# Kernel optimization log

Hardware: AMD Instinct MI355X
Metric: run time of the kernel (lower is better)

Reference implementation:

```python
import jax, jax.numpy as jnp
import numpy as np

ALPHA = 0.2          # LeakyReLU negative slope
NEG_INF = -9e15      # mask value from the original code


def setup_inputs() -> dict:
    key = jax.random.key(0)
    k1, k2, k3, k4 = jax.random.split(key, 4)
    B, N, F_in, F_out = 8, 2048, 64, 64
    x = jax.random.normal(k1, (B, N, F_in), dtype=jnp.float32)
    adj = jax.random.randint(k2, (B, N, N), 0, 2, dtype=jnp.int32)
    W = jax.random.normal(k3, (F_in, F_out), dtype=jnp.float32)
    a = jax.random.normal(k4, (2 * F_out, 1), dtype=jnp.float32)
    return {"x": x, "adj": adj, "W": W, "a": a}


def reference(x, adj, W, a):
    # h: [B, N, F_out]
    h = jnp.matmul(x, W)
    F_out = W.shape[1]
    a1 = a[:F_out, 0]   # source half of attention vector
    a2 = a[F_out:, 0]   # target half
    # e_ij = leakyrelu(h_i . a1 + h_j . a2)  -- identical math to the
    # original cat([h_i, h_j]) @ a without materializing [B,N*N,2F].
    s1 = jnp.einsum('bnf,f->bn', h, a1)  # [B, N]
    s2 = jnp.einsum('bnf,f->bn', h, a2)  # [B, N]
    e = jax.nn.leaky_relu(s1[:, :, None] + s2[:, None, :], negative_slope=ALPHA)
    masked = jnp.where(adj > 0, e, NEG_INF)
    attention = jax.nn.softmax(masked, axis=2)  # [B, N, N]
    # dropout p=0.0 / eval mode -> identity
    h_prime = jnp.matmul(attention, h)          # [B, N, F_out]
    return jax.nn.elu(h_prime)                  # concat=True branch
```

## Files before the change

### kernel.cpp

```cpp
#include <hip/hip_runtime.h>
#include <cstdint>

#define LRELU_ALPHA 0.2f
#define NEG_INF -9000000000000000.0f
#define L2E 1.4426950408889634f

typedef __bf16 bf16x8 __attribute__((ext_vector_type(8)));
typedef float floatx4 __attribute__((ext_vector_type(4)));

constexpr int Bb = 8, Nn = 2048, Ff = 64;
constexpr int SEG = 16;
constexpr int SEGJ = Nn / SEG;
constexpr int NROWS = Bb * Nn;
constexpr int LSTR2 = 136;

__device__ __forceinline__ unsigned f2bf_u(float f) {
    unsigned u = __builtin_bit_cast(unsigned, f);
    return u + 0x7FFFu + ((u >> 16) & 1u);
}
__device__ __forceinline__ unsigned short f2bf(float f) {
    return (unsigned short)(f2bf_u(f) >> 16);
}
__device__ __forceinline__ unsigned pkbf(float lo, float hi) {
    return (f2bf_u(lo) >> 16) | (f2bf_u(hi) & 0xFFFF0000u);
}

__global__ __launch_bounds__(256) void gat_pack(
    const int* __restrict__ adj, unsigned long long* __restrict__ amask)
{
    const int lane = threadIdx.x & 63;
    const int w    = threadIdx.x >> 6;
    const long long wave_id = (long long)blockIdx.x * 4 + w;
    const long long c0 = wave_id * 8;
    #pragma unroll
    for (int it = 0; it < 8; ++it) {
        const long long chunk = c0 + it;
        const int4 v = reinterpret_cast<const int4*>(adj + chunk * 256)[lane];
        const unsigned long long b0 = __ballot(v.x > 0);
        const unsigned long long b1 = __ballot(v.y > 0);
        const unsigned long long b2 = __ballot(v.z > 0);
        const unsigned long long b3 = __ballot(v.w > 0);
        if (lane == 0) {
            ulonglong2* o = reinterpret_cast<ulonglong2*>(amask + chunk * 4);
            o[0] = ulonglong2{b0, b1};
            o[1] = ulonglong2{b2, b3};
        }
    }
}

__global__ __launch_bounds__(256) void gat_prep(
    const float* __restrict__ x, const float* __restrict__ W, const float* __restrict__ a,
    unsigned short* __restrict__ hT, float* __restrict__ s1g, float* __restrict__ s2g)
{
    constexpr int STR2 = 36;
    __shared__ unsigned short hblk[64 * STR2];
    const int tid = threadIdx.x;
    const int blk = blockIdx.x;
    const int b  = blk >> 6;
    const int i0 = (blk & 63) * 32;
    const int w    = tid >> 6;
    const int lane = tid & 63;

    float wcol[64];
    #pragma unroll
    for (int k = 0; k < 64; ++k) wcol[k] = W[k * 64 + lane];
    const float a1 = a[lane], a2 = a[64 + lane];

    for (int r = 0; r < 8; ++r) {
        const int il = w * 8 + r;
        const int i  = i0 + il;
        const float* xrow = x + ((size_t)(b * Nn + i)) * 64;
        float h = 0.f;
        #pragma unroll
        for (int k = 0; k < 64; ++k) h = fmaf(xrow[k], wcol[k], h);
        float p1 = h * a1, p2 = h * a2;
        #pragma unroll
        for (int off = 32; off; off >>= 1) {
            p1 += __shfl_xor(p1, off);
            p2 += __shfl_xor(p2, off);
        }
        if (lane == 0) { s1g[b * Nn + i] = p1 * L2E; s2g[b * Nn + i] = p2 * L2E; }
        hblk[lane * STR2 + il] = f2bf(h);
    }
    __syncthreads();
    {
        const int f = tid >> 2, c = (tid & 3) * 8;
        uint4 v = *reinterpret_cast<const uint4*>(&hblk[f * STR2 + c]);
        *reinterpret_cast<uint4*>(hT + ((size_t)b * 64 + f) * Nn + i0 + c) = v;
    }
}

__global__ __launch_bounds__(256, 5) void gat_attn(
    const unsigned long long* __restrict__ amask, const unsigned short* __restrict__ hT,
    const float* __restrict__ s1g, const float* __restrict__ s2g,
    float* __restrict__ m_part, float* __restrict__ l_part, float* __restrict__ O_part)
{
    __shared__ __align__(16) char smem[64 * LSTR2 * 2];
    __shared__ float s2_lds[SEGJ];
    unsigned short* hT_lds = reinterpret_cast<unsigned short*>(smem);
    float* out_lds = reinterpret_cast<float*>(smem);

    const int tid  = threadIdx.x;
    const int blk  = blockIdx.x;
    const int seg  = blk >> 8;
    const int grp  = blk & 255;
    const int gr0  = grp * 64;
    const int b    = gr0 >> 11;
    const int i0   = gr0 & 2047;
    const int w    = tid >> 6;
    const int lane = tid & 63;
    const int fl   = lane & 15;
    const int q    = lane >> 4;

    const int i = i0 + w * 16 + fl;
    const float s1v = s1g[b * Nn + i];
    const unsigned short* hTb = hT + (size_t)b * 64 * Nn;
    const int jseg0 = seg * SEGJ;

    unsigned w32[4];
    {
        const unsigned long long* mrow =
            amask + (size_t)(b * Nn + i) * 32 + (seg >> 1) * 4;
        ulonglong2 m01 = reinterpret_cast<const ulonglong2*>(mrow)[0];
        ulonglong2 m23 = reinterpret_cast<const ulonglong2*>(mrow)[1];
        const int sh = (seg & 1) * 32 + q * 2;
        w32[0] = (unsigned)(m01.x >> sh);
        w32[1] = (unsigned)(m01.y >> sh);
        w32[2] = (unsigned)(m23.x >> sh);
        w32[3] = (unsigned)(m23.y >> sh);
    }

    #pragma unroll
    for (int k = 0; k < 4; ++k) {
        const int fr = k * 16 + (tid >> 4);
        const int c  = (tid & 15) * 8;
        uint4 v = *reinterpret_cast<const uint4*>(hTb + (size_t)fr * Nn + jseg0 + c);
        *reinterpret_cast<uint4*>(&hT_lds[fr * LSTR2 + c]) = v;
    }
    if (tid < SEGJ) s2_lds[tid] = s2g[b * Nn + jseg0 + tid];
    __syncthreads();

    float e[32];
    #pragma unroll
    for (int T = 0; T < 2; ++T) {
        #pragma unroll
        for (int H = 0; H < 2; ++H) {
            float s2v[8];
            *reinterpret_cast<float4*>(&s2v[0]) =
                *reinterpret_cast<const float4*>(&s2_lds[T * 64 + H * 32 + q * 8]);
            *reinterpret_cast<float4*>(&s2v[4]) =
                *reinterpret_cast<const float4*>(&s2_lds[T * 64 + H * 32 + q * 8 + 4]);
            #pragma unroll
            for (int jj = 0; jj < 8; ++jj) {
                float ev = s1v + s2v[jj];
                ev = fmaxf(ev, LRELU_ALPHA * ev);
                const bool on = (w32[jj & 3] >> (T * 16 + H * 8 + (jj >> 2))) & 1u;
                e[T * 16 + H * 8 + jj] = on ? ev : NEG_INF;
            }
        }
    }

    float m = e[0];
    #pragma unroll
    for (int k = 1; k < 32; ++k) m = fmaxf(m, e[k]);
    m = fmaxf(m, __shfl_xor(m, 16));
    m = fmaxf(m, __shfl_xor(m, 32));

    float l = 0.f;
    #pragma unroll
    for (int k = 0; k < 32; ++k) {
        e[k] = exp2f(e[k] - m);
        l += e[k];
    }
    l += __shfl_xor(l, 16);
    l += __shfl_xor(l, 32);

    floatx4 C[4] = {};
    #pragma unroll
    for (int T = 0; T < 2; ++T) {
        uint4 pl0, pl1;
        pl0.x = pkbf(e[T*16+0], e[T*16+1]);  pl0.y = pkbf(e[T*16+2], e[T*16+3]);
        pl0.z = pkbf(e[T*16+4], e[T*16+5]);  pl0.w = pkbf(e[T*16+6], e[T*16+7]);
        pl1.x = pkbf(e[T*16+8], e[T*16+9]);  pl1.y = pkbf(e[T*16+10], e[T*16+11]);
        pl1.z = pkbf(e[T*16+12], e[T*16+13]); pl1.w = pkbf(e[T*16+14], e[T*16+15]);
        const bf16x8 A0 = __builtin_bit_cast(bf16x8, pl0);
        const bf16x8 A1 = __builtin_bit_cast(bf16x8, pl1);
        #pragma unroll
        for (int u = 0; u < 4; ++u) {
            const bf16x8 B0 = *reinterpret_cast<const bf16x8*>(
                &hT_lds[(u * 16 + fl) * LSTR2 + T * 64 + q * 8]);
            C[u] = __builtin_amdgcn_mfma_f32_16x16x32_bf16(A0, B0, C[u], 0, 0, 0);
            const bf16x8 B1 = *reinterpret_cast<const bf16x8*>(
                &hT_lds[(u * 16 + fl) * LSTR2 + T * 64 + 32 + q * 8]);
            C[u] = __builtin_amdgcn_mfma_f32_16x16x32_bf16(A1, B1, C[u], 0, 0, 0);
        }
    }

    if (q == 0) {
        const int ri = b * Nn + i;
        m_part[seg * NROWS + ri] = m;
        l_part[seg * NROWS + ri] = l;
    }

    __syncthreads();
    #pragma unroll
    for (int u = 0; u < 4; ++u)
        #pragma unroll
        for (int r = 0; r < 4; ++r)
            out_lds[(w * 16 + q * 4 + r) * 65 + u * 16 + fl] = C[u][r];
    __syncthreads();
    {
        float* Obase = O_part + ((size_t)seg * NROWS + b * Nn + i0) * 64;
        #pragma unroll
        for (int k = 0; k < 4; ++k) {
            const int row = k * 16 + (tid >> 4);
            const int c4  = (tid & 15) * 4;
            float4 v = *reinterpret_cast<const float4*>(&out_lds[row * 65 + c4]);
            *reinterpret_cast<float4*>(&Obase[(size_t)row * 64 + c4]) = v;
        }
    }
}

__global__ __launch_bounds__(256) void gat_merge(
    const float* __restrict__ m_part, const float* __restrict__ l_part,
    const float* __restrict__ O_part, float* __restrict__ out)
{
    const int tid = threadIdx.x;
    const int ri  = blockIdx.x * 4 + (tid >> 6);
    const int f   = tid & 63;

    float mv[SEG];
    #pragma unroll
    for (int s = 0; s < SEG; ++s) mv[s] = m_part[s * NROWS + ri];
    float mstar = mv[0];
    #pragma unroll
    for (int s = 1; s < SEG; ++s) mstar = fmaxf(mstar, mv[s]);

    float lsum = 0.f, acc = 0.f;
    #pragma unroll
    for (int s = 0; s < SEG; ++s) {
        const float wgt = exp2f(mv[s] - mstar);
        lsum += l_part[s * NROWS + ri] * wgt;
        acc  += O_part[((size_t)s * NROWS + ri) * 64 + f] * wgt;
    }
    float v = acc / lsum;
    v = (v > 0.f) ? v : (exp2f(v * L2E) - 1.f);
    out[(size_t)ri * 64 + f] = v;
}

extern "C" void kernel_launch(void* const* d_in, const int* in_sizes, int n_in,
                              void* d_out, int out_size, void* d_ws, size_t ws_size,
                              hipStream_t stream) {
    const float* x   = (const float*)d_in[0];
    const int*   adj = (const int*)d_in[1];
    const float* W   = (const float*)d_in[2];
    const float* a   = (const float*)d_in[3];
    float* out = (float*)d_out;

    char* p = (char*)d_ws;
    unsigned short* hT = (unsigned short*)p;  p += (size_t)Bb * 64 * Nn * sizeof(unsigned short);
    float* s1 = (float*)p;                    p += (size_t)NROWS * sizeof(float);
    float* s2 = (float*)p;                    p += (size_t)NROWS * sizeof(float);
    float* m_part = (float*)p;                p += (size_t)SEG * NROWS * sizeof(float);
    float* l_part = (float*)p;                p += (size_t)SEG * NROWS * sizeof(float);
    float* O_part = (float*)p;                p += (size_t)SEG * NROWS * 64 * sizeof(float);
    unsigned long long* amask = (unsigned long long*)p;

    gat_pack<<<dim3(4096), dim3(256), 0, stream>>>(adj, amask);
    gat_prep<<<dim3(Bb * Nn / 32), dim3(256), 0, stream>>>(x, W, a, hT, s1, s2);
    gat_attn<<<dim3(SEG * (Bb * Nn / 64)), dim3(256), 0, stream>>>(
        amask, hT, s1, s2, m_part, l_part, O_part);
    gat_merge<<<dim3(NROWS / 4), dim3(256), 0, stream>>>(m_part, l_part, O_part, out);
}
```

Before: 256.1 us.

## Store partial outputs in bf16 and read hT/s2 directly from global memory

The attention kernel no longer stages the hT tile and s2 values in LDS. It loads MFMA B operands and s2 straight from global memory, which drops a barrier and most of the LDS use. Partial output accumulators are written as bf16 instead of fp32, halving the O_part write and the merge read traffic, and the occupancy hint changes from 5 to 4. The cost is strided, uncoalesced global loads for the B operands and reduced precision in the partial sums.

```diff
diff --git a/kernel.cpp b/kernel.cpp
--- a/kernel.cpp
+++ b/kernel.cpp
@@ -12,7 +12,6 @@
 constexpr int SEG = 16;
 constexpr int SEGJ = Nn / SEG;
 constexpr int NROWS = Bb * Nn;
-constexpr int LSTR2 = 136;
 
 __device__ __forceinline__ unsigned f2bf_u(float f) {
     unsigned u = __builtin_bit_cast(unsigned, f);
@@ -23,6 +22,9 @@
 }
 __device__ __forceinline__ unsigned pkbf(float lo, float hi) {
     return (f2bf_u(lo) >> 16) | (f2bf_u(hi) & 0xFFFF0000u);
+}
+__device__ __forceinline__ float bf2f(unsigned short b) {
+    return __builtin_bit_cast(float, (unsigned)b << 16);
 }
 
 __global__ __launch_bounds__(256) void gat_pack(
@@ -90,15 +92,13 @@
     }
 }
 
-__global__ __launch_bounds__(256, 5) void gat_attn(
+__global__ __launch_bounds__(256, 4) void gat_attn(
     const unsigned long long* __restrict__ amask, const unsigned short* __restrict__ hT,
     const float* __restrict__ s1g, const float* __restrict__ s2g,
-    float* __restrict__ m_part, float* __restrict__ l_part, float* __restrict__ O_part)
-{
-    __shared__ __align__(16) char smem[64 * LSTR2 * 2];
-    __shared__ float s2_lds[SEGJ];
-    unsigned short* hT_lds = reinterpret_cast<unsigned short*>(smem);
-    float* out_lds = reinterpret_cast<float*>(smem);
+    float* __restrict__ m_part, float* __restrict__ l_part,
+    unsigned short* __restrict__ O_part)
+{
+    __shared__ unsigned short out_lds[64 * 68];
 
     const int tid  = threadIdx.x;
     const int blk  = blockIdx.x;
@@ -115,6 +115,7 @@
     const int i = i0 + w * 16 + fl;
     const float s1v = s1g[b * Nn + i];
     const unsigned short* hTb = hT + (size_t)b * 64 * Nn;
+    const float* s2b = s2g + b * Nn;
     const int jseg0 = seg * SEGJ;
 
     unsigned w32[4];
@@ -130,16 +131,6 @@
         w32[3] = (unsigned)(m23.y >> sh);
     }
 
-    #pragma unroll
-    for (int k = 0; k < 4; ++k) {
-        const int fr = k * 16 + (tid >> 4);
-        const int c  = (tid & 15) * 8;
-        uint4 v = *reinterpret_cast<const uint4*>(hTb + (size_t)fr * Nn + jseg0 + c);
-        *reinterpret_cast<uint4*>(&hT_lds[fr * LSTR2 + c]) = v;
-    }
-    if (tid < SEGJ) s2_lds[tid] = s2g[b * Nn + jseg0 + tid];
-    __syncthreads();
-
     float e[32];
     #pragma unroll
     for (int T = 0; T < 2; ++T) {
@@ -147,9 +138,9 @@
         for (int H = 0; H < 2; ++H) {
             float s2v[8];
             *reinterpret_cast<float4*>(&s2v[0]) =
-                *reinterpret_cast<const float4*>(&s2_lds[T * 64 + H * 32 + q * 8]);
+                *reinterpret_cast<const float4*>(&s2b[jseg0 + T * 64 + H * 32 + q * 8]);
             *reinterpret_cast<float4*>(&s2v[4]) =
-                *reinterpret_cast<const float4*>(&s2_lds[T * 64 + H * 32 + q * 8 + 4]);
+                *reinterpret_cast<const float4*>(&s2b[jseg0 + T * 64 + H * 32 + q * 8 + 4]);
             #pragma unroll
             for (int jj = 0; jj < 8; ++jj) {
                 float ev = s1v + s2v[jj];
@@ -175,6 +166,7 @@
     l += __shfl_xor(l, 16);
     l += __shfl_xor(l, 32);
 
+    const unsigned short* hrow = hTb + (size_t)fl * Nn + jseg0 + q * 8;
     floatx4 C[4] = {};
     #pragma unroll
     for (int T = 0; T < 2; ++T) {
@@ -188,10 +180,10 @@
         #pragma unroll
         for (int u = 0; u < 4; ++u) {
             const bf16x8 B0 = *reinterpret_cast<const bf16x8*>(
-                &hT_lds[(u * 16 + fl) * LSTR2 + T * 64 + q * 8]);
+                hrow + (size_t)u * 16 * Nn + T * 64);
             C[u] = __builtin_amdgcn_mfma_f32_16x16x32_bf16(A0, B0, C[u], 0, 0, 0);
             const bf16x8 B1 = *reinterpret_cast<const bf16x8*>(
-                &hT_lds[(u * 16 + fl) * LSTR2 + T * 64 + 32 + q * 8]);
+                hrow + (size_t)u * 16 * Nn + T * 64 + 32);
             C[u] = __builtin_amdgcn_mfma_f32_16x16x32_bf16(A1, B1, C[u], 0, 0, 0);
         }
     }
@@ -202,28 +194,27 @@
         l_part[seg * NROWS + ri] = l;
     }
 
-    __syncthreads();
     #pragma unroll
     for (int u = 0; u < 4; ++u)
         #pragma unroll
         for (int r = 0; r < 4; ++r)
-            out_lds[(w * 16 + q * 4 + r) * 65 + u * 16 + fl] = C[u][r];
+            out_lds[(w * 16 + q * 4 + r) * 68 + u * 16 + fl] = f2bf(C[u][r]);
     __syncthreads();
     {
-        float* Obase = O_part + ((size_t)seg * NROWS + b * Nn + i0) * 64;
-        #pragma unroll
-        for (int k = 0; k < 4; ++k) {
-            const int row = k * 16 + (tid >> 4);
-            const int c4  = (tid & 15) * 4;
-            float4 v = *reinterpret_cast<const float4*>(&out_lds[row * 65 + c4]);
-            *reinterpret_cast<float4*>(&Obase[(size_t)row * 64 + c4]) = v;
+        unsigned short* Obase = O_part + ((size_t)seg * NROWS + b * Nn + i0) * 64;
+        #pragma unroll
+        for (int k = 0; k < 2; ++k) {
+            const int row = k * 32 + (tid >> 3);
+            const int c8  = (tid & 7) * 8;
+            uint4 v = *reinterpret_cast<const uint4*>(&out_lds[row * 68 + c8]);
+            *reinterpret_cast<uint4*>(&Obase[(size_t)row * 64 + c8]) = v;
         }
     }
 }
 
 __global__ __launch_bounds__(256) void gat_merge(
     const float* __restrict__ m_part, const float* __restrict__ l_part,
-    const float* __restrict__ O_part, float* __restrict__ out)
+    const unsigned short* __restrict__ O_part, float* __restrict__ out)
 {
     const int tid = threadIdx.x;
     const int ri  = blockIdx.x * 4 + (tid >> 6);
@@ -241,7 +232,7 @@
     for (int s = 0; s < SEG; ++s) {
         const float wgt = exp2f(mv[s] - mstar);
         lsum += l_part[s * NROWS + ri] * wgt;
-        acc  += O_part[((size_t)s * NROWS + ri) * 64 + f] * wgt;
+        acc  += bf2f(O_part[((size_t)s * NROWS + ri) * 64 + f]) * wgt;
     }
     float v = acc / lsum;
     v = (v > 0.f) ? v : (exp2f(v * L2E) - 1.f);
@@ -263,7 +254,8 @@
     float* s2 = (float*)p;                    p += (size_t)NROWS * sizeof(float);
     float* m_part = (float*)p;                p += (size_t)SEG * NROWS * sizeof(float);
     float* l_part = (float*)p;                p += (size_t)SEG * NROWS * sizeof(float);
-    float* O_part = (float*)p;                p += (size_t)SEG * NROWS * 64 * sizeof(float);
+    unsigned short* O_part = (unsigned short*)p;
+    p += (size_t)SEG * NROWS * 64 * sizeof(unsigned short);
     unsigned long long* amask = (unsigned long long*)p;
 
     gat_pack<<<dim3(4096), dim3(256), 0, stream>>>(adj, amask);
```

Measured after the change: 262.9 us. 1.03x slower.
